# Kernel optimization log

Measured on AMD Instinct MI355X. Metric: run time of the kernel, lower is better.

The kernel has to match this reference:

```python
import jax, jax.numpy as jnp
import numpy as np

B, TQ, TY = 8, 400, 400
Q_DIM, Y_DIM, ATT_DIM = 256, 256, 128


def setup_inputs() -> dict:
    key = jax.random.key(0)
    ks = jax.random.split(key, 9)
    s_q = 1.0 / np.sqrt(Q_DIM)
    s_y = 1.0 / np.sqrt(Y_DIM)
    s_a = 1.0 / np.sqrt(ATT_DIM)
    return {
        "query": jax.random.normal(ks[0], (B, TQ, Q_DIM), jnp.float32),
        "y": jax.random.normal(ks[1], (B, TY, Y_DIM), jnp.float32),
        "Wq_w": jax.random.uniform(ks[2], (ATT_DIM, Q_DIM), jnp.float32, -s_q, s_q),
        "Wq_b": jax.random.uniform(ks[3], (ATT_DIM,), jnp.float32, -s_q, s_q),
        "Wy_w": jax.random.uniform(ks[4], (ATT_DIM, Y_DIM), jnp.float32, -s_y, s_y),
        "Wy_b": jax.random.uniform(ks[5], (ATT_DIM,), jnp.float32, -s_y, s_y),
        "v_w": jax.random.uniform(ks[6], (1, ATT_DIM), jnp.float32, -s_a, s_a),
        "v_b": jax.random.uniform(ks[7], (1,), jnp.float32, -s_a, s_a),
        "n_wins_y": jax.random.randint(ks[8], (B,), TY // 2, TY + 1, jnp.int64 if jax.config.jax_enable_x64 else jnp.int32),
    }


def reference(query, y, Wq_w, Wq_b, Wy_w, Wy_b, v_w, v_b, n_wins_y):
    # Bahdanau scores: tanh(Wq(q)[:,None,:,:] + Wy(y)[:,:,None,:]) -> [B,Ty,Tq,A]
    q_proj = jnp.einsum('bqd,ad->bqa', query, Wq_w) + Wq_b      # [B,Tq,A]
    y_proj = jnp.einsum('btd,ad->bta', y, Wy_w) + Wy_b          # [B,Ty,A]
    h = jnp.tanh(q_proj[:, None, :, :] + y_proj[:, :, None, :])  # [B,Ty,Tq,A]
    att = jnp.einsum('btqa,a->btq', h, v_w[0]) + v_b[0]          # [B,Ty,Tq]
    att = jnp.transpose(att, (0, 2, 1))                          # [B,Tq,Ty]
    # mask invalid y windows (dim 2 = Ty), then softmax over Ty
    mask = jnp.arange(att.shape[2])[None, None, :] < n_wins_y[:, None, None]
    att = jnp.where(mask, att, -jnp.inf)
    att = jax.nn.softmax(att, axis=2)
    # soft attention apply: bmm(att, y) -> [B,Tq,y_dim]
    return jnp.einsum('bqt,btd->bqd', att, y)
```

## Files before the change

kernel.cpp:

```cpp
#include <hip/hip_runtime.h>


#define LOG2E 1.4426950408889634f
#define TANH_SCALE 2.8853900817779268f

constexpr int TQn = 400, TYn = 400, AD = 128, DD = 256;
constexpr int PTS = 12;

__global__ __launch_bounds__(128) void transpose_kernel(
    const float* __restrict__ Wq, const float* __restrict__ Wy,
    const float* __restrict__ vw,
    float4* __restrict__ WTq, float4* __restrict__ WTy,
    float* __restrict__ vneg)
{
    const int k4 = blockIdx.x & 63;
    const bool isq = blockIdx.x < 64;
    const float4* src = reinterpret_cast<const float4*>(isq ? Wq : Wy);
    float4* dst = isq ? WTq : WTy;
    const int a = threadIdx.x;
    dst[k4 * 128 + a] = src[a * 64 + k4];
    if (blockIdx.x == 0) vneg[a] = -2.f * vw[a];
}

__global__ __launch_bounds__(256, 4) void proj_kernel(
    const float* __restrict__ qin, const float* __restrict__ yin,
    const float4* __restrict__ WTq, const float* __restrict__ bq,
    const float4* __restrict__ WTy, const float* __restrict__ by,
    float* __restrict__ EqS, float* __restrict__ EyT)
{
    const int blk = blockIdx.x;
    const bool is_q = blk < 800;
    const int row0 = (is_q ? blk : blk - 800) * 4;
    const float* in   = (is_q ? qin : yin) + (size_t)row0 * DD;
    const float4* wt  = is_q ? WTq : WTy;
    const float* bias = is_q ? bq : by;

    __shared__ float lin[4 * DD];
    __shared__ float red[4][AD];
    {
        const float4* in4 = reinterpret_cast<const float4*>(in);
        reinterpret_cast<float4*>(lin)[threadIdx.x] = in4[threadIdx.x];
    }
    __syncthreads();

    const int a = threadIdx.x & 127;
    const int h = threadIdx.x >> 7;
    float acc[4] = {0.f, 0.f, 0.f, 0.f};
    const float4* l4 = reinterpret_cast<const float4*>(lin);
    #pragma unroll 8
    for (int i = 0; i < 32; ++i) {
        const int k4 = h * 32 + i;
        float4 w4 = wt[k4 * 128 + a];
        #pragma unroll
        for (int r = 0; r < 4; ++r) {
            float4 v = l4[r * 64 + k4];
            acc[r] = fmaf(w4.x, v.x, acc[r]);
            acc[r] = fmaf(w4.y, v.y, acc[r]);
            acc[r] = fmaf(w4.z, v.z, acc[r]);
            acc[r] = fmaf(w4.w, v.w, acc[r]);
        }
    }
    if (h) {
        #pragma unroll
        for (int r = 0; r < 4; ++r) red[r][a] = acc[r];
    }
    __syncthreads();
    if (!h) {
        const float bb = bias[a];
        const int a4 = a >> 2, ac = a & 3;
        const int qoff = (row0 & 7);
        #pragma unroll
        for (int r = 0; r < 4; ++r) {
            const float e = __builtin_amdgcn_exp2f(
                (acc[r] + red[r][a] + bb) * TANH_SCALE);
            if (is_q)
                EqS[(size_t)(row0 >> 3) * 1024 + a4 * 32 + (qoff + r) * 4 + ac] = e;
            else
                EyT[(size_t)a4 * 12800 + (size_t)(row0 + r) * 4 + ac] = e;
        }
    }
}

__global__ __launch_bounds__(448, 2) void score_kernel(
    const float* __restrict__ EqS,
    const float4* __restrict__ EyT4,
    const float* __restrict__ vneg,
    const int*  __restrict__ nwins,
    float* __restrict__ s)
{
    const int grp = blockIdx.x;
    const int b   = grp / 100;
    const int qg  = grp % 100;
    const int q0  = qg * 4;
    const int n   = nwins[b];
    const int t   = threadIdx.x;
    if ((t & ~63) >= n) return;

    const int ycol = b * TYn + min(t, TYn - 1);
    const float4* eqg = reinterpret_cast<const float4*>(EqS)
                      + (size_t)(b * 50 + (qg >> 1)) * 256 + 4 * (qg & 1);
    const float4* vn4 = reinterpret_cast<const float4*>(vneg);

    float ac0 = 0.f, ac1 = 0.f, ac2 = 0.f, ac3 = 0.f;
    for (int a4 = 0; a4 < 32; ++a4) {
        const float4 ey = EyT4[(size_t)a4 * 3200 + ycol];
        const float4* eqa = eqg + a4 * 8;
        const float4 vv = vn4[a4];
        const float4 e0 = eqa[0], e1 = eqa[1], e2 = eqa[2], e3 = eqa[3];
        #define SCORE_Q(ACC, EQ)                                            \
        {                                                                   \
            float a0 = fmaf(EQ.x, ey.x, 1.f);                               \
            float a1 = fmaf(EQ.y, ey.y, 1.f);                               \
            float a2 = fmaf(EQ.z, ey.z, 1.f);                               \
            float a3 = fmaf(EQ.w, ey.w, 1.f);                               \
            float p01 = a0 * a1, p23 = a2 * a3;                             \
            float R = __builtin_amdgcn_rcpf(p01 * p23);                     \
            float u = p23 * R, w = p01 * R;                                 \
            ACC = fmaf(vv.x, a1 * u, ACC);                                  \
            ACC = fmaf(vv.y, a0 * u, ACC);                                  \
            ACC = fmaf(vv.z, a3 * w, ACC);                                  \
            ACC = fmaf(vv.w, a2 * w, ACC);                                  \
        }
        SCORE_Q(ac0, e0) SCORE_Q(ac1, e1) SCORE_Q(ac2, e2) SCORE_Q(ac3, e3)
        #undef SCORE_Q
    }
    if (t < n) {
        float* srow = s + (size_t)(b * TQn + q0) * TYn + t;
        srow[0 * TYn] = ac0; srow[1 * TYn] = ac1;
        srow[2 * TYn] = ac2; srow[3 * TYn] = ac3;
    }
}

__global__ __launch_bounds__(512, 2) void apply_kernel(
    const float* __restrict__ y,
    const float* __restrict__ s,
    const int*  __restrict__ nwins,
    float* __restrict__ out)
{
    const int bid = blockIdx.x;
    const int b   = bid / 50;
    const int q0  = (bid % 50) * 8;
    const int tid = threadIdx.x, wave = tid >> 6, lane = tid & 63;
    const int n = nwins[b];
    const float NEG_INF = -__builtin_inff();

    __shared__ __align__(16) float4 s_buf4[1200];
    float* s_pT = reinterpret_cast<float*>(s_buf4);

    const float* srow = s + (size_t)(b * TQn + q0 + wave) * TYn;
    float sc0, sc1, sc2, sc3, sc4, sc5, sc6;
    {
        int t;
        t = 0 * 64 + lane; sc0 = (t < n) ? srow[t] : NEG_INF;
        t = 1 * 64 + lane; sc1 = (t < n) ? srow[t] : NEG_INF;
        t = 2 * 64 + lane; sc2 = (t < n) ? srow[t] : NEG_INF;
        t = 3 * 64 + lane; sc3 = (t < n) ? srow[t] : NEG_INF;
        t = 4 * 64 + lane; sc4 = (t < n) ? srow[t] : NEG_INF;
        t = 5 * 64 + lane; sc5 = (t < n) ? srow[t] : NEG_INF;
        t = 6 * 64 + lane; sc6 = (t < n) ? srow[t] : NEG_INF;
    }
    float m = fmaxf(fmaxf(fmaxf(sc0, sc1), fmaxf(sc2, sc3)),
                    fmaxf(fmaxf(sc4, sc5), sc6));
    #pragma unroll
    for (int off = 32; off >= 1; off >>= 1) m = fmaxf(m, __shfl_xor(m, off, 64));
    sc0 = __builtin_amdgcn_exp2f((sc0 - m) * LOG2E);
    sc1 = __builtin_amdgcn_exp2f((sc1 - m) * LOG2E);
    sc2 = __builtin_amdgcn_exp2f((sc2 - m) * LOG2E);
    sc3 = __builtin_amdgcn_exp2f((sc3 - m) * LOG2E);
    sc4 = __builtin_amdgcn_exp2f((sc4 - m) * LOG2E);
    sc5 = __builtin_amdgcn_exp2f((sc5 - m) * LOG2E);
    sc6 = __builtin_amdgcn_exp2f((sc6 - m) * LOG2E);
    float l = ((sc0 + sc1) + (sc2 + sc3)) + ((sc4 + sc5) + sc6);
    #pragma unroll
    for (int off = 32; off >= 1; off >>= 1) l += __shfl_xor(l, off, 64);
    const float inv = 1.0f / l;
    s_pT[(0 * 64 + lane) * PTS + wave] = sc0 * inv;
    s_pT[(1 * 64 + lane) * PTS + wave] = sc1 * inv;
    s_pT[(2 * 64 + lane) * PTS + wave] = sc2 * inv;
    s_pT[(3 * 64 + lane) * PTS + wave] = sc3 * inv;
    s_pT[(4 * 64 + lane) * PTS + wave] = sc4 * inv;
    s_pT[(5 * 64 + lane) * PTS + wave] = sc5 * inv;
    {
        const int t = 6 * 64 + lane;
        if (t < TYn) s_pT[t * PTS + wave] = sc6 * inv;
    }
    __syncthreads();

    const float4* yb4 = reinterpret_cast<const float4*>(y) + (size_t)(b * TYn) * 64;
    float4 ac0 = {0,0,0,0}, ac1 = {0,0,0,0}, ac2 = {0,0,0,0}, ac3 = {0,0,0,0};
    float4 ac4 = {0,0,0,0}, ac5 = {0,0,0,0}, ac6 = {0,0,0,0}, ac7 = {0,0,0,0};

    int tA = wave;
    float4 yA = yb4[(size_t)tA * 64 + lane];
    float4 pa_A = *reinterpret_cast<const float4*>(&s_pT[tA * PTS]);
    float4 pb_A = *reinterpret_cast<const float4*>(&s_pT[tA * PTS + 4]);
    int tB = wave + 8;
    float4 yB = yb4[(size_t)tB * 64 + lane];
    float4 pa_B = *reinterpret_cast<const float4*>(&s_pT[tB * PTS]);
    float4 pb_B = *reinterpret_cast<const float4*>(&s_pT[tB * PTS + 4]);

    #define ACCUM(PA, PB, YV)                                               \
        ac0.x = fmaf(PA.x, YV.x, ac0.x); ac0.y = fmaf(PA.x, YV.y, ac0.y);   \
        ac0.z = fmaf(PA.x, YV.z, ac0.z); ac0.w = fmaf(PA.x, YV.w, ac0.w);   \
        ac1.x = fmaf(PA.y, YV.x, ac1.x); ac1.y = fmaf(PA.y, YV.y, ac1.y);   \
        ac1.z = fmaf(PA.y, YV.z, ac1.z); ac1.w = fmaf(PA.y, YV.w, ac1.w);   \
        ac2.x = fmaf(PA.z, YV.x, ac2.x); ac2.y = fmaf(PA.z, YV.y, ac2.y);   \
        ac2.z = fmaf(PA.z, YV.z, ac2.z); ac2.w = fmaf(PA.z, YV.w, ac2.w);   \
        ac3.x = fmaf(PA.w, YV.x, ac3.x); ac3.y = fmaf(PA.w, YV.y, ac3.y);   \
        ac3.z = fmaf(PA.w, YV.z, ac3.z); ac3.w = fmaf(PA.w, YV.w, ac3.w);   \
        ac4.x = fmaf(PB.x, YV.x, ac4.x); ac4.y = fmaf(PB.x, YV.y, ac4.y);   \
        ac4.z = fmaf(PB.x, YV.z, ac4.z); ac4.w = fmaf(PB.x, YV.w, ac4.w);   \
        ac5.x = fmaf(PB.y, YV.x, ac5.x); ac5.y = fmaf(PB.y, YV.y, ac5.y);   \
        ac5.z = fmaf(PB.y, YV.z, ac5.z); ac5.w = fmaf(PB.y, YV.w, ac5.w);   \
        ac6.x = fmaf(PB.z, YV.x, ac6.x); ac6.y = fmaf(PB.z, YV.y, ac6.y);   \
        ac6.z = fmaf(PB.z, YV.z, ac6.z); ac6.w = fmaf(PB.z, YV.w, ac6.w);   \
        ac7.x = fmaf(PB.w, YV.x, ac7.x); ac7.y = fmaf(PB.w, YV.y, ac7.y);   \
        ac7.z = fmaf(PB.w, YV.z, ac7.z); ac7.w = fmaf(PB.w, YV.w, ac7.w);

    for (int i = 0; i < 25; ++i) {
        {
            const float4 pa = pa_A, pb = pb_A, yv = yA;
            const int tn = tA + 16;
            if (i < 24) {
                yA = yb4[(size_t)tn * 64 + lane];
                pa_A = *reinterpret_cast<const float4*>(&s_pT[tn * PTS]);
                pb_A = *reinterpret_cast<const float4*>(&s_pT[tn * PTS + 4]);
                tA = tn;
            }
            ACCUM(pa, pb, yv)
        }
        {
            const float4 pa = pa_B, pb = pb_B, yv = yB;
            const int tn = tB + 16;
            if (i < 24) {
                yB = yb4[(size_t)tn * 64 + lane];
                pa_B = *reinterpret_cast<const float4*>(&s_pT[tn * PTS]);
                pb_B = *reinterpret_cast<const float4*>(&s_pT[tn * PTS + 4]);
                tB = tn;
            }
            ACCUM(pa, pb, yv)
        }
    }
    #undef ACCUM

    float4* rbuf = s_buf4;
    float4* o4 = reinterpret_cast<float4*>(out) + (size_t)(b * TQn + q0) * 64;
    auto rphase = [&](float4 AQ, float4 BQ, int PH) {
        __syncthreads();
        rbuf[wave * 128 + lane]      = AQ;
        rbuf[wave * 128 + 64 + lane] = BQ;
        __syncthreads();
        if (tid < 128) {
            const int qi = tid >> 6, dr = tid & 63;
            float4 s0 = rbuf[0 * 128 + qi * 64 + dr];
            #pragma unroll
            for (int w2 = 1; w2 < 8; ++w2) {
                float4 v = rbuf[w2 * 128 + qi * 64 + dr];
                s0.x += v.x; s0.y += v.y; s0.z += v.z; s0.w += v.w;
            }
            o4[(size_t)(PH * 2 + qi) * 64 + dr] = s0;
        }
    };
    rphase(ac0, ac1, 0);
    rphase(ac2, ac3, 1);
    rphase(ac4, ac5, 2);
    rphase(ac6, ac7, 3);
}

extern "C" void kernel_launch(void* const* d_in, const int* in_sizes, int n_in,
                              void* d_out, int out_size, void* d_ws, size_t ws_size,
                              hipStream_t stream) {
    const float* query = (const float*)d_in[0];
    const float* y     = (const float*)d_in[1];
    const float* Wq_w  = (const float*)d_in[2];
    const float* Wq_b  = (const float*)d_in[3];
    const float* Wy_w  = (const float*)d_in[4];
    const float* Wy_b  = (const float*)d_in[5];
    const float* v_w   = (const float*)d_in[6];
    const int* nw      = (const int*)d_in[8];
    float* out = (float*)d_out;

    float4* WTq  = (float4*)d_ws;
    float4* WTy  = WTq + 64 * 128;
    float*  vneg = (float*)(WTy + 64 * 128);
    float*  EqS  = vneg + 256;
    float*  EyT  = EqS + (size_t)400 * 1024;
    float*  s    = EyT + (size_t)32 * 3200 * 4;

    transpose_kernel<<<128, 128, 0, stream>>>(Wq_w, Wy_w, v_w, WTq, WTy, vneg);
    proj_kernel<<<1600, 256, 0, stream>>>(query, y, WTq, Wq_b, WTy, Wy_b, EqS, EyT);
    score_kernel<<<8 * 100, 448, 0, stream>>>(
        EqS, (const float4*)EyT, vneg, nw, s);
    apply_kernel<<<8 * 50, 512, 0, stream>>>(y, s, nw, out);
}
```

Before: 60.29 us.

## Split apply kernel across two column halves to double block count

The apply kernel now launches 800 blocks instead of 400, each handling half of the 256 output columns for its 8 query rows. Within a wave, the two 32-lane halves process different t rows, so each wave covers 2 t per step and keeps one prefetch chain instead of two. The final reduction sums both lane halves across the 8 waves. The softmax over each score row is now recomputed twice, once per column-half block. The occupancy hint is raised to 4 blocks per unit, which caps register use per thread.

```diff
diff --git a/kernel.cpp b/kernel.cpp
--- a/kernel.cpp
+++ b/kernel.cpp
@@ -131,15 +131,18 @@
     }
 }
 
-__global__ __launch_bounds__(512, 2) void apply_kernel(
+__global__ __launch_bounds__(512, 4) void apply_kernel(
     const float* __restrict__ y,
     const float* __restrict__ s,
     const int*  __restrict__ nwins,
     float* __restrict__ out)
 {
     const int bid = blockIdx.x;
-    const int b   = bid / 50;
-    const int q0  = (bid % 50) * 8;
+    const int b   = bid / 100;
+    const int rem = bid % 100;
+    const int qg  = rem >> 1;
+    const int dh  = rem & 1;
+    const int q0  = qg * 8;
     const int tid = threadIdx.x, wave = tid >> 6, lane = tid & 63;
     const int n = nwins[b];
     const float NEG_INF = -__builtin_inff();
@@ -186,77 +189,61 @@
     }
     __syncthreads();
 
+    const int col = dh * 32 + (lane & 31);
+    const int rp  = lane >> 5;
     const float4* yb4 = reinterpret_cast<const float4*>(y) + (size_t)(b * TYn) * 64;
     float4 ac0 = {0,0,0,0}, ac1 = {0,0,0,0}, ac2 = {0,0,0,0}, ac3 = {0,0,0,0};
     float4 ac4 = {0,0,0,0}, ac5 = {0,0,0,0}, ac6 = {0,0,0,0}, ac7 = {0,0,0,0};
 
-    int tA = wave;
-    float4 yA = yb4[(size_t)tA * 64 + lane];
-    float4 pa_A = *reinterpret_cast<const float4*>(&s_pT[tA * PTS]);
-    float4 pb_A = *reinterpret_cast<const float4*>(&s_pT[tA * PTS + 4]);
-    int tB = wave + 8;
-    float4 yB = yb4[(size_t)tB * 64 + lane];
-    float4 pa_B = *reinterpret_cast<const float4*>(&s_pT[tB * PTS]);
-    float4 pb_B = *reinterpret_cast<const float4*>(&s_pT[tB * PTS + 4]);
-
-    #define ACCUM(PA, PB, YV)                                               \
-        ac0.x = fmaf(PA.x, YV.x, ac0.x); ac0.y = fmaf(PA.x, YV.y, ac0.y);   \
-        ac0.z = fmaf(PA.x, YV.z, ac0.z); ac0.w = fmaf(PA.x, YV.w, ac0.w);   \
-        ac1.x = fmaf(PA.y, YV.x, ac1.x); ac1.y = fmaf(PA.y, YV.y, ac1.y);   \
-        ac1.z = fmaf(PA.y, YV.z, ac1.z); ac1.w = fmaf(PA.y, YV.w, ac1.w);   \
-        ac2.x = fmaf(PA.z, YV.x, ac2.x); ac2.y = fmaf(PA.z, YV.y, ac2.y);   \
-        ac2.z = fmaf(PA.z, YV.z, ac2.z); ac2.w = fmaf(PA.z, YV.w, ac2.w);   \
-        ac3.x = fmaf(PA.w, YV.x, ac3.x); ac3.y = fmaf(PA.w, YV.y, ac3.y);   \
-        ac3.z = fmaf(PA.w, YV.z, ac3.z); ac3.w = fmaf(PA.w, YV.w, ac3.w);   \
-        ac4.x = fmaf(PB.x, YV.x, ac4.x); ac4.y = fmaf(PB.x, YV.y, ac4.y);   \
-        ac4.z = fmaf(PB.x, YV.z, ac4.z); ac4.w = fmaf(PB.x, YV.w, ac4.w);   \
-        ac5.x = fmaf(PB.y, YV.x, ac5.x); ac5.y = fmaf(PB.y, YV.y, ac5.y);   \
-        ac5.z = fmaf(PB.y, YV.z, ac5.z); ac5.w = fmaf(PB.y, YV.w, ac5.w);   \
-        ac6.x = fmaf(PB.z, YV.x, ac6.x); ac6.y = fmaf(PB.z, YV.y, ac6.y);   \
-        ac6.z = fmaf(PB.z, YV.z, ac6.z); ac6.w = fmaf(PB.z, YV.w, ac6.w);   \
-        ac7.x = fmaf(PB.w, YV.x, ac7.x); ac7.y = fmaf(PB.w, YV.y, ac7.y);   \
-        ac7.z = fmaf(PB.w, YV.z, ac7.z); ac7.w = fmaf(PB.w, YV.w, ac7.w);
+    int r = 2 * wave + rp;
+    float4 yv = yb4[(size_t)r * 64 + col];
+    float4 pa = *reinterpret_cast<const float4*>(&s_pT[r * PTS]);
+    float4 pb = *reinterpret_cast<const float4*>(&s_pT[r * PTS + 4]);
 
     for (int i = 0; i < 25; ++i) {
-        {
-            const float4 pa = pa_A, pb = pb_A, yv = yA;
-            const int tn = tA + 16;
-            if (i < 24) {
-                yA = yb4[(size_t)tn * 64 + lane];
-                pa_A = *reinterpret_cast<const float4*>(&s_pT[tn * PTS]);
-                pb_A = *reinterpret_cast<const float4*>(&s_pT[tn * PTS + 4]);
-                tA = tn;
-            }
-            ACCUM(pa, pb, yv)
-        }
-        {
-            const float4 pa = pa_B, pb = pb_B, yv = yB;
-            const int tn = tB + 16;
-            if (i < 24) {
-                yB = yb4[(size_t)tn * 64 + lane];
-                pa_B = *reinterpret_cast<const float4*>(&s_pT[tn * PTS]);
-                pb_B = *reinterpret_cast<const float4*>(&s_pT[tn * PTS + 4]);
-                tB = tn;
-            }
-            ACCUM(pa, pb, yv)
-        }
-    }
-    #undef ACCUM
+        const float4 yc = yv, pac = pa, pbc = pb;
+        if (i < 24) {
+            const int rn = r + 16;
+            yv = yb4[(size_t)rn * 64 + col];
+            pa = *reinterpret_cast<const float4*>(&s_pT[rn * PTS]);
+            pb = *reinterpret_cast<const float4*>(&s_pT[rn * PTS + 4]);
+            r = rn;
+        }
+        ac0.x = fmaf(pac.x, yc.x, ac0.x); ac0.y = fmaf(pac.x, yc.y, ac0.y);
+        ac0.z = fmaf(pac.x, yc.z, ac0.z); ac0.w = fmaf(pac.x, yc.w, ac0.w);
+        ac1.x = fmaf(pac.y, yc.x, ac1.x); ac1.y = fmaf(pac.y, yc.y, ac1.y);
+        ac1.z = fmaf(pac.y, yc.z, ac1.z); ac1.w = fmaf(pac.y, yc.w, ac1.w);
+        ac2.x = fmaf(pac.z, yc.x, ac2.x); ac2.y = fmaf(pac.z, yc.y, ac2.y);
+        ac2.z = fmaf(pac.z, yc.z, ac2.z); ac2.w = fmaf(pac.z, yc.w, ac2.w);
+        ac3.x = fmaf(pac.w, yc.x, ac3.x); ac3.y = fmaf(pac.w, yc.y, ac3.y);
+        ac3.z = fmaf(pac.w, yc.z, ac3.z); ac3.w = fmaf(pac.w, yc.w, ac3.w);
+        ac4.x = fmaf(pbc.x, yc.x, ac4.x); ac4.y = fmaf(pbc.x, yc.y, ac4.y);
+        ac4.z = fmaf(pbc.x, yc.z, ac4.z); ac4.w = fmaf(pbc.x, yc.w, ac4.w);
+        ac5.x = fmaf(pbc.y, yc.x, ac5.x); ac5.y = fmaf(pbc.y, yc.y, ac5.y);
+        ac5.z = fmaf(pbc.y, yc.z, ac5.z); ac5.w = fmaf(pbc.y, yc.w, ac5.w);
+        ac6.x = fmaf(pbc.z, yc.x, ac6.x); ac6.y = fmaf(pbc.z, yc.y, ac6.y);
+        ac6.z = fmaf(pbc.z, yc.z, ac6.z); ac6.w = fmaf(pbc.z, yc.w, ac6.w);
+        ac7.x = fmaf(pbc.w, yc.x, ac7.x); ac7.y = fmaf(pbc.w, yc.y, ac7.y);
+        ac7.z = fmaf(pbc.w, yc.z, ac7.z); ac7.w = fmaf(pbc.w, yc.w, ac7.w);
+    }
 
     float4* rbuf = s_buf4;
-    float4* o4 = reinterpret_cast<float4*>(out) + (size_t)(b * TQn + q0) * 64;
+    float4* o4 = reinterpret_cast<float4*>(out)
+               + (size_t)(b * TQn + q0) * 64 + dh * 32;
     auto rphase = [&](float4 AQ, float4 BQ, int PH) {
         __syncthreads();
         rbuf[wave * 128 + lane]      = AQ;
         rbuf[wave * 128 + 64 + lane] = BQ;
         __syncthreads();
-        if (tid < 128) {
-            const int qi = tid >> 6, dr = tid & 63;
-            float4 s0 = rbuf[0 * 128 + qi * 64 + dr];
+        if (tid < 64) {
+            const int qi = tid >> 5, dr = tid & 31;
+            float4 s0 = {0.f, 0.f, 0.f, 0.f};
             #pragma unroll
-            for (int w2 = 1; w2 < 8; ++w2) {
-                float4 v = rbuf[w2 * 128 + qi * 64 + dr];
-                s0.x += v.x; s0.y += v.y; s0.z += v.z; s0.w += v.w;
+            for (int w2 = 0; w2 < 8; ++w2) {
+                float4 va = rbuf[w2 * 128 + qi * 64 + dr];
+                float4 vb = rbuf[w2 * 128 + qi * 64 + 32 + dr];
+                s0.x += va.x + vb.x; s0.y += va.y + vb.y;
+                s0.z += va.z + vb.z; s0.w += va.w + vb.w;
             }
             o4[(size_t)(PH * 2 + qi) * 64 + dr] = s0;
         }
@@ -291,5 +278,5 @@
     proj_kernel<<<1600, 256, 0, stream>>>(query, y, WTq, Wq_b, WTy, Wy_b, EqS, EyT);
     score_kernel<<<8 * 100, 448, 0, stream>>>(
         EqS, (const float4*)EyT, vneg, nw, s);
-    apply_kernel<<<8 * 50, 512, 0, stream>>>(y, s, nw, out);
-}
+    apply_kernel<<<8 * 100, 512, 0, stream>>>(y, s, nw, out);
+}
```

New measurement: 63.88 us. +6.0%, slower.
